# Kernel tuning notes

Measured on AMD Instinct MI355X. Metric: run time of the kernel, lower is better.

Reference implementation:

```python
import jax, jax.numpy as jnp
import numpy as np


def setup_inputs() -> dict:
    key = jax.random.key(0)
    ks = jax.random.split(key, 8)
    B, L, D, H = 4, 2048, 4096, 8
    BW = D // H
    std = 1.0 / np.sqrt(BW)
    x = jax.random.normal(ks[0], (B, L, D), dtype=jnp.float32)
    segment_pos = jax.random.randint(ks[1], (B, L), 0, 1024)
    prev_h = jax.random.normal(ks[2], (B, D), dtype=jnp.float32)
    w_in = jax.random.normal(ks[3], (H, BW, BW), dtype=jnp.float32) * std
    b_in = jnp.zeros((H, BW), dtype=jnp.float32)
    w_a = jax.random.normal(ks[4], (H, BW, BW), dtype=jnp.float32) * std
    b_a = jnp.zeros((H, BW), dtype=jnp.float32)
    # a_param init: uniform on ring [0.9, 0.999], softplus-inverse transform
    unif = jax.random.uniform(ks[5], (D,), dtype=jnp.float32)
    min_rad, max_rad = 0.9, 0.999
    a_real = 0.5 * jnp.log(unif * (max_rad**2 - min_rad**2) + min_rad**2 + 1e-8)
    a_param = jnp.log(jnp.exp(-a_real) - 1.0)
    return {"x": x, "segment_pos": segment_pos, "prev_h": prev_h,
            "w_in": w_in, "b_in": b_in, "w_a": w_a, "b_a": b_a,
            "a_param": a_param}


def _block_diag_linear(x, w, b):
    # x: [B,L,D]; w: [H,BW,BW]; b: [H,BW]
    B, L, D = x.shape
    H = w.shape[0]
    xr = x.reshape(B, L, H, D // H)
    y = jnp.einsum('blhi,hij->blhj', xr, w) + b
    return y.reshape(B, L, D)


def reference(x, segment_pos, prev_h, w_in, b_in, w_a, b_a, a_param):
    # reset indicator at document boundaries (segment_pos == 0)
    reset = (segment_pos == 0).astype(x.dtype)          # [B,L]
    gate_x = jax.nn.sigmoid(_block_diag_linear(x, w_in, b_in))
    gate_a = jax.nn.sigmoid(_block_diag_linear(x, w_a, b_a))
    log_a = -8.0 * gate_a * jax.nn.softplus(a_param)    # [B,L,D]
    a = jnp.exp(log_a)
    multiplier = jnp.sqrt(1.0 - jnp.exp(2.0 * log_a) + 1e-6)
    multiplier = reset[..., None] + (1.0 - reset)[..., None] * multiplier
    normalized_x = x * gate_x * multiplier
    # zero the decay at reset positions (hidden state reset)
    a = a * (1.0 - reset)[..., None]
    # linear recurrence y_t = a_t * y_{t-1} + x_t (initial hidden state = 0,
    # matching the torch L>1 path which does not use prev_h)
    def combine(c1, c2):
        a1, b1 = c1
        a2, b2 = c2
        return (a2 * a1, a2 * b1 + b2)
    _, y = jax.lax.associative_scan(combine, (a, normalized_x), axis=1)
    return y
```

## Files before the change

kernel.cpp:

```cpp
#include <hip/hip_runtime.h>
#include <hip/hip_bf16.h>

typedef _Float16 f16;
typedef _Float16 f16x2 __attribute__((ext_vector_type(2)));
typedef _Float16 f16x4 __attribute__((ext_vector_type(4)));
typedef _Float16 f16x8 __attribute__((ext_vector_type(8)));
typedef float f32x4 __attribute__((ext_vector_type(4)));

#define B_  4
#define L_  2048
#define D_  4096
#define H_  8
#define BW_ 512
#define M_  (B_*L_)
#define CHUNK 128
#define NCH (L_/CHUNK)
#define LOG2E 1.4426950408889634f

static const size_t OFF_WPK   = 0;
static const size_t OFF_MSP   = 8ull<<20;
static const size_t OFF_XH    = 9ull<<20;
static const size_t OFF_YLAP  = 73ull<<20;
static const size_t OFF_SUMA  = 208ull<<20;
static const size_t OFF_SUMY  = 209ull<<20;
static const size_t OFF_CARRY = 210ull<<20;

__device__ __forceinline__ void gl16(const void* g, void* l) {
    __builtin_amdgcn_global_load_lds(
        (const __attribute__((address_space(1))) unsigned int*)g,
        (__attribute__((address_space(3))) unsigned int*)l, 16, 0, 0);
}

__global__ __launch_bounds__(256)
void prep_wpack(const float* __restrict__ w_in, const float* __restrict__ w_a,
                f16* __restrict__ wpk) {
    const int kt  = blockIdx.x & 7;
    const int n32 = (blockIdx.x >> 3) & 15;
    const int h   = blockIdx.x >> 7;
    const int tid = threadIdx.x;
#pragma unroll
    for (int q = 0; q < 2; ++q) {
        int slot = q * 256 + tid;
        int lane = slot & 63;
        int fidx = slot >> 6;
        int g    = fidx >> 2;
        int fn   = (fidx >> 1) & 1;
        int kk2  = fidx & 1;
        int row = n32 * 32 + fn * 16 + (lane & 15);
        int col = kt * 64 + kk2 * 32 + ((lane >> 4) << 3);
        const float* src = (g ? w_a : w_in) + (size_t)h * BW_ * BW_;
        f16x8 v;
#pragma unroll
        for (int e = 0; e < 8; ++e)
            v[e] = (f16)src[(size_t)(col + e) * BW_ + row];
        size_t o = ((((size_t)(h * 16 + n32) * 8 + kt) * 8) + fidx) * 64 + lane;
        *(f16x8*)(wpk + o * 8) = v;
    }
}

__global__ __launch_bounds__(256)
void prep_msp(const float* __restrict__ a_param, float* __restrict__ msp2) {
    int d = blockIdx.x * 256 + threadIdx.x;
    float v = a_param[d];
    msp2[d] = -8.f * log1pf(expf(v)) * LOG2E;
}

__global__ __launch_bounds__(256)
void prep_xh(const float* __restrict__ x, f16* __restrict__ xh) {
    size_t i = ((size_t)blockIdx.x * 256 + threadIdx.x) * 8;
    size_t stride = (size_t)gridDim.x * 256 * 8;
    for (; i < (size_t)M_ * D_; i += stride) {
        f32x4 v0 = *(const f32x4*)(x + i);
        f32x4 v1 = *(const f32x4*)(x + i + 4);
        f16x8 hv;
        hv[0] = (f16)v0.x; hv[1] = (f16)v0.y; hv[2] = (f16)v0.z; hv[3] = (f16)v0.w;
        hv[4] = (f16)v1.x; hv[5] = (f16)v1.y; hv[6] = (f16)v1.z; hv[7] = (f16)v1.w;
        *(f16x8*)(xh + i) = hv;
    }
}

#define BM 128
#define BN 64
#define BKK 64
#define NT (BW_/BKK)
#define BUFB 16384

#define SMEM_BYTES 52992

__global__ __launch_bounds__(256, 3)
void gemm_gates(const f16*   __restrict__ xh,
                const int*   __restrict__ segpos,
                const f16*   __restrict__ wpk,
                const float* __restrict__ b_in,
                const float* __restrict__ b_a,
                const float* __restrict__ msp2,
                f16x2* __restrict__ ylap,
                float* __restrict__ sumA,
                float* __restrict__ sumY) {
    __shared__ __align__(16) char smem[SMEM_BYTES];
    float* a_s  = (float*)smem;
    f16*   xn_s = (f16*)(smem + 33280);
    float* segA = (float*)(smem + 50176);
    float* segY = (float*)(smem + 51328);
    float* rst_s= (float*)(smem + 52480);

    const int tid  = threadIdx.x;
    const int m0   = blockIdx.x * BM;
    const int n0   = blockIdx.y * BN;
    const int h    = blockIdx.z;
    const int lane = tid & 63;
    const int wid  = tid >> 6;
    const int wr   = wid >> 1;
    const int wc   = wid & 1;

    f32x4 accX[4][2] = {};
    f32x4 accA[4][2] = {};

    if (tid < BM) rst_s[tid] = (segpos[m0 + tid] == 0) ? 1.f : 0.f;

    const int grow  = lane >> 3;
    const int gcolS = (((lane & 7) ^ grow) << 3);
    const f16* aSrc = xh + (size_t)(m0 + wid * 32 + grow) * D_ + h * BW_ + gcolS;

    const f16* wbase = wpk + ((size_t)(h * 16) + (n0 >> 5) + wc) * 32768;

    const int swz  = (lane & 7) << 3;
    const int kx   = (lane >> 4) << 3;
    const int arow = wr * 64 + (lane & 15);

    const int rowb = wr * 64 + ((lane >> 4) << 2);
    const int txo = (n0 >> 6) + 1;

    f16x8 bfr[2][8];

    {
        const int k0 = (txo & (NT - 1)) * BKK;
        f16* Asb = (f16*)smem;
#pragma unroll
        for (int q = 0; q < 4; ++q)
            gl16(aSrc + k0 + (size_t)q * 8 * D_, &Asb[(wid * 32 + q * 8) * 64]);
        const f16* tp = wbase + (size_t)(txo & (NT - 1)) * 4096;
#pragma unroll
        for (int j = 0; j < 8; ++j)
            bfr[0][j] = *(const f16x8*)(tp + j * 512 + lane * 8);
    }

#pragma unroll
    for (int t = 0; t < NT; ++t) {
        const int cur = t & 1;
        if (t + 1 < NT) {
            const int kt1 = (t + 1 + txo) & (NT - 1);
            f16* Asb = (f16*)(smem + (cur ^ 1) * BUFB);
#pragma unroll
            for (int q = 0; q < 4; ++q)
                gl16(aSrc + kt1 * BKK + (size_t)q * 8 * D_, &Asb[(wid * 32 + q * 8) * 64]);
            const f16* tp = wbase + (size_t)kt1 * 4096;
#pragma unroll
            for (int j = 0; j < 8; ++j)
                bfr[cur ^ 1][j] = *(const f16x8*)(tp + j * 512 + lane * 8);
            asm volatile("s_waitcnt vmcnt(12)" ::: "memory");
        } else {
            asm volatile("s_waitcnt vmcnt(0)" ::: "memory");
        }
        __builtin_amdgcn_s_barrier();
        __builtin_amdgcn_sched_barrier(0);

        const f16* Asb = (const f16*)(smem + cur * BUFB);
#pragma unroll
        for (int kk2 = 0; kk2 < 2; ++kk2) {
            const int kcolS = (kk2 * 32 + kx) ^ swz;
            f16x8 af[4];
#pragma unroll
            for (int fm = 0; fm < 4; ++fm)
                af[fm] = *(const f16x8*)&Asb[(arow + fm * 16) * 64 + kcolS];
#pragma unroll
            for (int fn = 0; fn < 2; ++fn) {
                f16x8 bx = bfr[cur][fn * 2 + kk2];
                f16x8 ba = bfr[cur][4 + fn * 2 + kk2];
#pragma unroll
                for (int fm = 0; fm < 4; ++fm) {
                    accX[fm][fn] = __builtin_amdgcn_mfma_f32_16x16x32_f16(af[fm], bx, accX[fm][fn], 0, 0, 0);
                    accA[fm][fn] = __builtin_amdgcn_mfma_f32_16x16x32_f16(af[fm], ba, accA[fm][fn], 0, 0, 0);
                }
            }
        }
        __builtin_amdgcn_sched_barrier(0);
        __builtin_amdgcn_s_barrier();
    }

    const f16* As1 = (const f16*)(smem + BUFB);
    f16 xvv[2][4][4];
#pragma unroll
    for (int fn = 0; fn < 2; ++fn) {
        const int ctile = wc * 32 + fn * 16 + (lane & 15);
#pragma unroll
        for (int fm = 0; fm < 4; ++fm)
#pragma unroll
            for (int reg = 0; reg < 4; ++reg) {
                const int rowt = rowb + fm * 16 + reg;
                xvv[fn][fm][reg] = As1[rowt * 64 + (ctile ^ ((rowt & 7) << 3))];
            }
    }
    __syncthreads();

    {
#pragma unroll
        for (int fn = 0; fn < 2; ++fn) {
            const int ctile = wc * 32 + fn * 16 + (lane & 15);
            const int d = h * BW_ + n0 + ctile;
            const float bx = b_in[d];
            const float ba = b_a[d];
            const float mspd = msp2[d];
#pragma unroll
            for (int fm = 0; fm < 4; ++fm) {
#pragma unroll
                for (int reg = 0; reg < 4; ++reg) {
                    const int rowt = rowb + fm * 16 + reg;
                    float gxl = accX[fm][fn][reg] + bx;
                    float gal = accA[fm][fn][reg] + ba;
                    float gx = __builtin_amdgcn_rcpf(1.f + __builtin_amdgcn_exp2f(-gxl * LOG2E));
                    float ga = __builtin_amdgcn_rcpf(1.f + __builtin_amdgcn_exp2f(-gal * LOG2E));
                    float a  = __builtin_amdgcn_exp2f(mspd * ga);
                    float a2 = a * a;
                    float mult = __builtin_amdgcn_sqrtf(1.f + 1e-6f - a2);
                    float rv = rst_s[rowt];
                    a *= (1.f - rv);
                    mult = rv + (1.f - rv) * mult;
                    float xv = (float)xvv[fn][fm][reg];
                    a_s[rowt * 65 + ctile] = a;
                    xn_s[rowt * 66 + ctile] = (f16)(xv * gx * mult);
                }
            }
        }
    }
    __syncthreads();

    const int scol = tid & 63;
    const int sseg = tid >> 6;
    {
        float A = 1.f, yv = 0.f;
#pragma unroll 4
        for (int t = sseg * 32; t < sseg * 32 + 32; ++t) {
            float a  = a_s[t * 65 + scol];
            float xn = (float)xn_s[t * 66 + scol];
            yv = fmaf(a, yv, xn);
            A *= a;
        }
        segA[sseg * 72 + scol] = A;
        segY[sseg * 72 + scol] = yv;
    }
    __syncthreads();

    {
        float cy = 0.f, pA = 1.f;
        for (int s = 0; s < sseg; ++s) {
            float As_ = segA[s * 72 + scol];
            float Ys_ = segY[s * 72 + scol];
            cy = fmaf(As_, cy, Ys_);
            pA *= As_;
        }
        float Arun = 1.f, yv = cy;
        const size_t obase = (size_t)(m0 + sseg * 32) * D_ + h * BW_ + n0 + scol;
#pragma unroll 4
        for (int i = 0; i < 32; ++i) {
            const int t = sseg * 32 + i;
            float a  = a_s[t * 65 + scol];
            float xn = (float)xn_s[t * 66 + scol];
            yv = fmaf(a, yv, xn);
            Arun *= a;
            f16x2 p;
            p[0] = (f16)yv;
            p[1] = (f16)(pA * Arun);
            ylap[obase + (size_t)i * D_] = p;
        }
        if (sseg == 3) {
            const int bb = m0 >> 11;
            const int cc = (m0 & 2047) >> 7;
            size_t si = ((size_t)bb * NCH + cc) * D_ + h * BW_ + n0 + scol;
            sumA[si] = pA * Arun;
            sumY[si] = yv;
        }
    }
}

__global__ __launch_bounds__(256)
void scan_mid(const float* __restrict__ sumA, const float* __restrict__ sumY,
              float* __restrict__ carry) {
    int d = blockIdx.x * 256 + threadIdx.x;
    int b = blockIdx.y;
    float hcur = 0.f;
#pragma unroll
    for (int c = 0; c < NCH; ++c) {
        size_t si = ((size_t)b * NCH + c) * D_ + d;
        carry[si] = hcur;
        hcur = fmaf(sumA[si], hcur, sumY[si]);
    }
}

__global__ __launch_bounds__(256)
void scan_apply(const float* __restrict__ carry, const f16x2* __restrict__ ylap,
                float* __restrict__ y) {
    size_t i4 = (size_t)blockIdx.x * 256 + threadIdx.x;
    const size_t stride = (size_t)gridDim.x * 256;
    const size_t n4 = (size_t)M_ * D_ / 4;
    for (; i4 < n4; i4 += stride) {
        size_t i = i4 * 4;
        size_t row = i >> 12;
        int d = (int)(i & 4095);
        int b = (int)(row >> 11);
        int c = ((int)row & 2047) >> 7;
        const float* cp = carry + (((size_t)(b * NCH + c)) << 12) + d;
        f32x4 cv = *(const f32x4*)cp;
        f16x8 pk = *(const f16x8*)(ylap + i);
        f32x4 o;
        o.x = fmaf(cv.x, (float)pk[1], (float)pk[0]);
        o.y = fmaf(cv.y, (float)pk[3], (float)pk[2]);
        o.z = fmaf(cv.z, (float)pk[5], (float)pk[4]);
        o.w = fmaf(cv.w, (float)pk[7], (float)pk[6]);
        *(f32x4*)(y + i) = o;
    }
}

extern "C" void kernel_launch(void* const* d_in, const int* in_sizes, int n_in,
                              void* d_out, int out_size, void* d_ws, size_t ws_size,
                              hipStream_t stream) {
    const float* x       = (const float*)d_in[0];
    const int*   segpos  = (const int*)d_in[1];
    const float* w_in    = (const float*)d_in[3];
    const float* b_in    = (const float*)d_in[4];
    const float* w_a     = (const float*)d_in[5];
    const float* b_a     = (const float*)d_in[6];
    const float* a_param = (const float*)d_in[7];

    float* y  = (float*)d_out;
    char*  ws = (char*)d_ws;
    f16*   wpk   = (f16*)(ws + OFF_WPK);
    float* msp2  = (float*)(ws + OFF_MSP);
    f16*   xh    = (f16*)(ws + OFF_XH);
    f16x2* ylap  = (f16x2*)(ws + OFF_YLAP);
    float* sumA  = (float*)(ws + OFF_SUMA);
    float* sumY  = (float*)(ws + OFF_SUMY);
    float* carry = (float*)(ws + OFF_CARRY);

    prep_wpack<<<dim3(1024), 256, 0, stream>>>(w_in, w_a, wpk);
    prep_msp<<<dim3(D_ / 256), 256, 0, stream>>>(a_param, msp2);
    prep_xh<<<dim3(2048), 256, 0, stream>>>(x, xh);
    gemm_gates<<<dim3(M_ / BM, BW_ / BN, H_), 256, 0, stream>>>(
        xh, segpos, wpk, b_in, b_a, msp2, ylap, sumA, sumY);
    scan_mid<<<dim3(D_ / 256, B_), 256, 0, stream>>>(sumA, sumY, carry);
    scan_apply<<<dim3(4096), 256, 0, stream>>>(carry, ylap, y);
}
```

Measured before the change: 223.5 us.

## Fuse chunk scan carry into GEMM via persistent decoupled-lookback chain

Measured after the change: 483.4 us. +116.3%, slower.

```diff
diff --git a/kernel.cpp b/kernel.cpp
--- a/kernel.cpp
+++ b/kernel.cpp
@@ -15,15 +15,16 @@
 #define M_  (B_*L_)
 #define CHUNK 128
 #define NCH (L_/CHUNK)
+#define NCHAINS 256
+#define NITEMS  4096
 #define LOG2E 1.4426950408889634f
 
 static const size_t OFF_WPK   = 0;
 static const size_t OFF_MSP   = 8ull<<20;
 static const size_t OFF_XH    = 9ull<<20;
-static const size_t OFF_YLAP  = 73ull<<20;
-static const size_t OFF_SUMA  = 208ull<<20;
-static const size_t OFF_SUMY  = 209ull<<20;
-static const size_t OFF_CARRY = 210ull<<20;
+static const size_t OFF_VALS  = 73ull<<20;
+static const size_t OFF_FLAGS = 74ull<<20;
+static const size_t OFF_CNT   = 75ull<<20;
 
 __device__ __forceinline__ void gl16(const void* g, void* l) {
     __builtin_amdgcn_global_load_lds(
@@ -79,131 +80,150 @@
     }
 }
 
+__global__ __launch_bounds__(256)
+void zero_sync(unsigned* __restrict__ flags, unsigned* __restrict__ counter) {
+    int i = blockIdx.x * 256 + threadIdx.x;
+    if (i < NITEMS) flags[i] = 0u;
+    if (i == 0) *counter = 0u;
+}
+
 #define BM 128
 #define BN 64
 #define BKK 64
 #define NT (BW_/BKK)
 #define BUFB 16384
 
-#define SMEM_BYTES 52992
+#define SMEM_BYTES 53504
 
 __global__ __launch_bounds__(256, 3)
-void gemm_gates(const f16*   __restrict__ xh,
+void gemm_chain(const f16*   __restrict__ xh,
                 const int*   __restrict__ segpos,
                 const f16*   __restrict__ wpk,
                 const float* __restrict__ b_in,
                 const float* __restrict__ b_a,
                 const float* __restrict__ msp2,
-                f16x2* __restrict__ ylap,
-                float* __restrict__ sumA,
-                float* __restrict__ sumY) {
+                unsigned* __restrict__ vals,
+                unsigned* __restrict__ flags,
+                unsigned* __restrict__ counter,
+                float* __restrict__ y) {
     __shared__ __align__(16) char smem[SMEM_BYTES];
-    float* a_s  = (float*)smem;
-    f16*   xn_s = (f16*)(smem + 33280);
-    float* segA = (float*)(smem + 50176);
-    float* segY = (float*)(smem + 51328);
-    float* rst_s= (float*)(smem + 52480);
+    float*    a_s   = (float*)smem;
+    f16*      xn_s  = (f16*)(smem + 33280);
+    float*    segA  = (float*)(smem + 50176);
+    float*    segY  = (float*)(smem + 51328);
+    float*    rst_s = (float*)(smem + 52480);
+    float*    h0_s  = (float*)(smem + 52992);
+    unsigned* tkt_s = (unsigned*)(smem + 53248);
 
     const int tid  = threadIdx.x;
-    const int m0   = blockIdx.x * BM;
-    const int n0   = blockIdx.y * BN;
-    const int h    = blockIdx.z;
     const int lane = tid & 63;
     const int wid  = tid >> 6;
     const int wr   = wid >> 1;
     const int wc   = wid & 1;
 
-    f32x4 accX[4][2] = {};
-    f32x4 accA[4][2] = {};
-
-    if (tid < BM) rst_s[tid] = (segpos[m0 + tid] == 0) ? 1.f : 0.f;
-
     const int grow  = lane >> 3;
     const int gcolS = (((lane & 7) ^ grow) << 3);
-    const f16* aSrc = xh + (size_t)(m0 + wid * 32 + grow) * D_ + h * BW_ + gcolS;
-
-    const f16* wbase = wpk + ((size_t)(h * 16) + (n0 >> 5) + wc) * 32768;
-
-    const int swz  = (lane & 7) << 3;
-    const int kx   = (lane >> 4) << 3;
-    const int arow = wr * 64 + (lane & 15);
-
-    const int rowb = wr * 64 + ((lane >> 4) << 2);
-    const int txo = (n0 >> 6) + 1;
-
-    f16x8 bfr[2][8];
-
-    {
-        const int k0 = (txo & (NT - 1)) * BKK;
-        f16* Asb = (f16*)smem;
-#pragma unroll
-        for (int q = 0; q < 4; ++q)
-            gl16(aSrc + k0 + (size_t)q * 8 * D_, &Asb[(wid * 32 + q * 8) * 64]);
-        const f16* tp = wbase + (size_t)(txo & (NT - 1)) * 4096;
-#pragma unroll
-        for (int j = 0; j < 8; ++j)
-            bfr[0][j] = *(const f16x8*)(tp + j * 512 + lane * 8);
-    }
-
-#pragma unroll
-    for (int t = 0; t < NT; ++t) {
-        const int cur = t & 1;
-        if (t + 1 < NT) {
-            const int kt1 = (t + 1 + txo) & (NT - 1);
-            f16* Asb = (f16*)(smem + (cur ^ 1) * BUFB);
+    const int swz   = (lane & 7) << 3;
+    const int kx    = (lane >> 4) << 3;
+    const int arow  = wr * 64 + (lane & 15);
+    const int rowb  = wr * 64 + ((lane >> 4) << 2);
+    const int scol  = tid & 63;
+    const int sseg  = tid >> 6;
+
+    for (;;) {
+        if (tid == 0) *tkt_s = atomicAdd(counter, 1u);
+        __syncthreads();
+        const unsigned item = *tkt_s;
+        if (item >= NITEMS) break;
+        const int cc    = item >> 8;
+        const int chain = item & 255;
+        const int bb    = chain >> 6;
+        const int h     = (chain >> 3) & 7;
+        const int nb    = chain & 7;
+        const int m0    = bb * L_ + cc * CHUNK;
+        const int n0    = nb * 64;
+
+        f32x4 accX[4][2] = {};
+        f32x4 accA[4][2] = {};
+
+        if (tid < BM) rst_s[tid] = (segpos[m0 + tid] == 0) ? 1.f : 0.f;
+
+        const f16* aSrc  = xh + (size_t)(m0 + wid * 32 + grow) * D_ + h * BW_ + gcolS;
+        const f16* wbase = wpk + ((size_t)(h * 16) + (n0 >> 5) + wc) * 32768;
+        const int  txo   = (n0 >> 6) + 1;
+
+        f16x8 bfr[2][8];
+
+        {
+            const int k0 = (txo & (NT - 1)) * BKK;
+            f16* Asb = (f16*)smem;
 #pragma unroll
             for (int q = 0; q < 4; ++q)
-                gl16(aSrc + kt1 * BKK + (size_t)q * 8 * D_, &Asb[(wid * 32 + q * 8) * 64]);
-            const f16* tp = wbase + (size_t)kt1 * 4096;
+                gl16(aSrc + k0 + (size_t)q * 8 * D_, &Asb[(wid * 32 + q * 8) * 64]);
+            const f16* tp = wbase + (size_t)(txo & (NT - 1)) * 4096;
 #pragma unroll
             for (int j = 0; j < 8; ++j)
-                bfr[cur ^ 1][j] = *(const f16x8*)(tp + j * 512 + lane * 8);
-            asm volatile("s_waitcnt vmcnt(12)" ::: "memory");
-        } else {
-            asm volatile("s_waitcnt vmcnt(0)" ::: "memory");
-        }
-        __builtin_amdgcn_s_barrier();
-        __builtin_amdgcn_sched_barrier(0);
-
-        const f16* Asb = (const f16*)(smem + cur * BUFB);
-#pragma unroll
-        for (int kk2 = 0; kk2 < 2; ++kk2) {
-            const int kcolS = (kk2 * 32 + kx) ^ swz;
-            f16x8 af[4];
+                bfr[0][j] = *(const f16x8*)(tp + j * 512 + lane * 8);
+        }
+
+#pragma unroll
+        for (int t = 0; t < NT; ++t) {
+            const int cur = t & 1;
+            if (t + 1 < NT) {
+                const int kt1 = (t + 1 + txo) & (NT - 1);
+                f16* Asb = (f16*)(smem + (cur ^ 1) * BUFB);
+#pragma unroll
+                for (int q = 0; q < 4; ++q)
+                    gl16(aSrc + kt1 * BKK + (size_t)q * 8 * D_, &Asb[(wid * 32 + q * 8) * 64]);
+                const f16* tp = wbase + (size_t)kt1 * 4096;
+#pragma unroll
+                for (int j = 0; j < 8; ++j)
+                    bfr[cur ^ 1][j] = *(const f16x8*)(tp + j * 512 + lane * 8);
+                asm volatile("s_waitcnt vmcnt(12)" ::: "memory");
+            } else {
+                asm volatile("s_waitcnt vmcnt(0)" ::: "memory");
+            }
+            __builtin_amdgcn_s_barrier();
+            __builtin_amdgcn_sched_barrier(0);
+
+            const f16* Asb = (const f16*)(smem + cur * BUFB);
+#pragma unroll
+            for (int kk2 = 0; kk2 < 2; ++kk2) {
+                const int kcolS = (kk2 * 32 + kx) ^ swz;
+                f16x8 af[4];
+#pragma unroll
+                for (int fm = 0; fm < 4; ++fm)
+                    af[fm] = *(const f16x8*)&Asb[(arow + fm * 16) * 64 + kcolS];
+#pragma unroll
+                for (int fn = 0; fn < 2; ++fn) {
+                    f16x8 bx = bfr[cur][fn * 2 + kk2];
+                    f16x8 ba = bfr[cur][4 + fn * 2 + kk2];
+#pragma unroll
+                    for (int fm = 0; fm < 4; ++fm) {
+                        accX[fm][fn] = __builtin_amdgcn_mfma_f32_16x16x32_f16(af[fm], bx, accX[fm][fn], 0, 0, 0);
+                        accA[fm][fn] = __builtin_amdgcn_mfma_f32_16x16x32_f16(af[fm], ba, accA[fm][fn], 0, 0, 0);
+                    }
+                }
+            }
+            __builtin_amdgcn_sched_barrier(0);
+            __builtin_amdgcn_s_barrier();
+        }
+
+        const f16* As1 = (const f16*)(smem + BUFB);
+        f16 xvv[2][4][4];
+#pragma unroll
+        for (int fn = 0; fn < 2; ++fn) {
+            const int ctile = wc * 32 + fn * 16 + (lane & 15);
 #pragma unroll
             for (int fm = 0; fm < 4; ++fm)
-                af[fm] = *(const f16x8*)&Asb[(arow + fm * 16) * 64 + kcolS];
-#pragma unroll
-            for (int fn = 0; fn < 2; ++fn) {
-                f16x8 bx = bfr[cur][fn * 2 + kk2];
-                f16x8 ba = bfr[cur][4 + fn * 2 + kk2];
-#pragma unroll
-                for (int fm = 0; fm < 4; ++fm) {
-                    accX[fm][fn] = __builtin_amdgcn_mfma_f32_16x16x32_f16(af[fm], bx, accX[fm][fn], 0, 0, 0);
-                    accA[fm][fn] = __builtin_amdgcn_mfma_f32_16x16x32_f16(af[fm], ba, accA[fm][fn], 0, 0, 0);
+#pragma unroll
+                for (int reg = 0; reg < 4; ++reg) {
+                    const int rowt = rowb + fm * 16 + reg;
+                    xvv[fn][fm][reg] = As1[rowt * 64 + (ctile ^ ((rowt & 7) << 3))];
                 }
-            }
-        }
-        __builtin_amdgcn_sched_barrier(0);
-        __builtin_amdgcn_s_barrier();
-    }
-
-    const f16* As1 = (const f16*)(smem + BUFB);
-    f16 xvv[2][4][4];
-#pragma unroll
-    for (int fn = 0; fn < 2; ++fn) {
-        const int ctile = wc * 32 + fn * 16 + (lane & 15);
-#pragma unroll
-        for (int fm = 0; fm < 4; ++fm)
-#pragma unroll
-            for (int reg = 0; reg < 4; ++reg) {
-                const int rowt = rowb + fm * 16 + reg;
-                xvv[fn][fm][reg] = As1[rowt * 64 + (ctile ^ ((rowt & 7) << 3))];
-            }
-    }
-    __syncthreads();
-
-    {
+        }
+        __syncthreads();
+
 #pragma unroll
         for (int fn = 0; fn < 2; ++fn) {
             const int ctile = wc * 32 + fn * 16 + (lane & 15);
@@ -232,92 +252,69 @@
                 }
             }
         }
-    }
-    __syncthreads();
-
-    const int scol = tid & 63;
-    const int sseg = tid >> 6;
-    {
-        float A = 1.f, yv = 0.f;
+        __syncthreads();
+
+        {
+            float A = 1.f, yv = 0.f;
 #pragma unroll 4
-        for (int t = sseg * 32; t < sseg * 32 + 32; ++t) {
-            float a  = a_s[t * 65 + scol];
-            float xn = (float)xn_s[t * 66 + scol];
-            yv = fmaf(a, yv, xn);
-            A *= a;
-        }
-        segA[sseg * 72 + scol] = A;
-        segY[sseg * 72 + scol] = yv;
-    }
-    __syncthreads();
-
-    {
-        float cy = 0.f, pA = 1.f;
-        for (int s = 0; s < sseg; ++s) {
-            float As_ = segA[s * 72 + scol];
-            float Ys_ = segY[s * 72 + scol];
-            cy = fmaf(As_, cy, Ys_);
-            pA *= As_;
-        }
-        float Arun = 1.f, yv = cy;
-        const size_t obase = (size_t)(m0 + sseg * 32) * D_ + h * BW_ + n0 + scol;
+            for (int t = sseg * 32; t < sseg * 32 + 32; ++t) {
+                float a  = a_s[t * 65 + scol];
+                float xn = (float)xn_s[t * 66 + scol];
+                yv = fmaf(a, yv, xn);
+                A *= a;
+            }
+            segA[sseg * 72 + scol] = A;
+            segY[sseg * 72 + scol] = yv;
+        }
+        __syncthreads();
+
+        if (tid < 64) {
+            float Af = 1.f, ye = 0.f;
+#pragma unroll
+            for (int s = 0; s < 4; ++s) {
+                float As_ = segA[s * 72 + tid];
+                ye = fmaf(As_, ye, segY[s * 72 + tid]);
+                Af *= As_;
+            }
+            float h0 = 0.f;
+            if (cc > 0) {
+                const unsigned* flg = flags + (item - NCHAINS);
+                while (__hip_atomic_load(flg, __ATOMIC_ACQUIRE,
+                                         __HIP_MEMORY_SCOPE_AGENT) == 0u)
+                    __builtin_amdgcn_s_sleep(2);
+                unsigned hv = __hip_atomic_load(
+                    vals + (size_t)(item - NCHAINS) * 64 + tid,
+                    __ATOMIC_RELAXED, __HIP_MEMORY_SCOPE_AGENT);
+                h0 = __uint_as_float(hv);
+            }
+            h0_s[tid] = h0;
+            float hend = fmaf(Af, h0, ye);
+            __hip_atomic_store(vals + (size_t)item * 64 + tid,
+                               __float_as_uint(hend),
+                               __ATOMIC_RELAXED, __HIP_MEMORY_SCOPE_AGENT);
+            asm volatile("s_waitcnt vmcnt(0)" ::: "memory");
+            __threadfence();
+            if (tid == 0)
+                __hip_atomic_store(flags + item, 1u,
+                                   __ATOMIC_RELEASE, __HIP_MEMORY_SCOPE_AGENT);
+        }
+        __syncthreads();
+
+        {
+            float cy = h0_s[scol];
+            for (int s = 0; s < sseg; ++s)
+                cy = fmaf(segA[s * 72 + scol], cy, segY[s * 72 + scol]);
+            float yv = cy;
+            const size_t obase = (size_t)(m0 + sseg * 32) * D_ + h * BW_ + n0 + scol;
 #pragma unroll 4
-        for (int i = 0; i < 32; ++i) {
-            const int t = sseg * 32 + i;
-            float a  = a_s[t * 65 + scol];
-            float xn = (float)xn_s[t * 66 + scol];
-            yv = fmaf(a, yv, xn);
-            Arun *= a;
-            f16x2 p;
-            p[0] = (f16)yv;
-            p[1] = (f16)(pA * Arun);
-            ylap[obase + (size_t)i * D_] = p;
-        }
-        if (sseg == 3) {
-            const int bb = m0 >> 11;
-            const int cc = (m0 & 2047) >> 7;
-            size_t si = ((size_t)bb * NCH + cc) * D_ + h * BW_ + n0 + scol;
-            sumA[si] = pA * Arun;
-            sumY[si] = yv;
-        }
-    }
-}
-
-__global__ __launch_bounds__(256)
-void scan_mid(const float* __restrict__ sumA, const float* __restrict__ sumY,
-              float* __restrict__ carry) {
-    int d = blockIdx.x * 256 + threadIdx.x;
-    int b = blockIdx.y;
-    float hcur = 0.f;
-#pragma unroll
-    for (int c = 0; c < NCH; ++c) {
-        size_t si = ((size_t)b * NCH + c) * D_ + d;
-        carry[si] = hcur;
-        hcur = fmaf(sumA[si], hcur, sumY[si]);
-    }
-}
-
-__global__ __launch_bounds__(256)
-void scan_apply(const float* __restrict__ carry, const f16x2* __restrict__ ylap,
-                float* __restrict__ y) {
-    size_t i4 = (size_t)blockIdx.x * 256 + threadIdx.x;
-    const size_t stride = (size_t)gridDim.x * 256;
-    const size_t n4 = (size_t)M_ * D_ / 4;
-    for (; i4 < n4; i4 += stride) {
-        size_t i = i4 * 4;
-        size_t row = i >> 12;
-        int d = (int)(i & 4095);
-        int b = (int)(row >> 11);
-        int c = ((int)row & 2047) >> 7;
-        const float* cp = carry + (((size_t)(b * NCH + c)) << 12) + d;
-        f32x4 cv = *(const f32x4*)cp;
-        f16x8 pk = *(const f16x8*)(ylap + i);
-        f32x4 o;
-        o.x = fmaf(cv.x, (float)pk[1], (float)pk[0]);
-        o.y = fmaf(cv.y, (float)pk[3], (float)pk[2]);
-        o.z = fmaf(cv.z, (float)pk[5], (float)pk[4]);
-        o.w = fmaf(cv.w, (float)pk[7], (float)pk[6]);
-        *(f32x4*)(y + i) = o;
+            for (int i = 0; i < 32; ++i) {
+                const int t = sseg * 32 + i;
+                float a  = a_s[t * 65 + scol];
+                float xn = (float)xn_s[t * 66 + scol];
+                yv = fmaf(a, yv, xn);
+                y[obase + (size_t)i * D_] = yv;
+            }
+        }
     }
 }
 
@@ -334,19 +331,17 @@
 
     float* y  = (float*)d_out;
     char*  ws = (char*)d_ws;
-    f16*   wpk   = (f16*)(ws + OFF_WPK);
-    float* msp2  = (float*)(ws + OFF_MSP);
-    f16*   xh    = (f16*)(ws + OFF_XH);
-    f16x2* ylap  = (f16x2*)(ws + OFF_YLAP);
-    float* sumA  = (float*)(ws + OFF_SUMA);
-    float* sumY  = (float*)(ws + OFF_SUMY);
-    float* carry = (float*)(ws + OFF_CARRY);
+    f16*      wpk   = (f16*)(ws + OFF_WPK);
+    float*    msp2  = (float*)(ws + OFF_MSP);
+    f16*      xh    = (f16*)(ws + OFF_XH);
+    unsigned* vals  = (unsigned*)(ws + OFF_VALS);
+    unsigned* flags = (unsigned*)(ws + OFF_FLAGS);
+    unsigned* cnt   = (unsigned*)(ws + OFF_CNT);
 
     prep_wpack<<<dim3(1024), 256, 0, stream>>>(w_in, w_a, wpk);
     prep_msp<<<dim3(D_ / 256), 256, 0, stream>>>(a_param, msp2);
+    zero_sync<<<dim3(NITEMS / 256), 256, 0, stream>>>(flags, cnt);
     prep_xh<<<dim3(2048), 256, 0, stream>>>(x, xh);
-    gemm_gates<<<dim3(M_ / BM, BW_ / BN, H_), 256, 0, stream>>>(
-        xh, segpos, wpk, b_in, b_a, msp2, ylap, sumA, sumY);
-    scan_mid<<<dim3(D_ / 256, B_), 256, 0, stream>>>(sumA, sumY, carry);
-    scan_apply<<<dim3(4096), 256, 0, stream>>>(carry, ylap, y);
-}
+    gemm_chain<<<dim3(768), 256, 0, stream>>>(
+        xh, segpos, wpk, b_in, b_a, msp2, vals, flags, cnt, y);
+}
```
